# Optimization experiments

Hardware: AMD Instinct MI355X
Metric: run time of the kernel (lower is better)

Reference implementation:

```python
import jax, jax.numpy as jnp
import numpy as np

B, S, DIN, DOUT = 2, 2048, 4096, 4096


def setup_inputs() -> dict:
    key = jax.random.key(0)
    k1, k2 = jax.random.split(key)
    x = jax.random.normal(k1, (B, S, DIN), dtype=jnp.float32)
    weight = jax.random.normal(k2, (DOUT, DIN), dtype=jnp.float32) * 0.02
    # xnor init for row scaling pattern
    mean = weight.mean(-1, keepdims=True)                      # [DOUT,1]
    scale = jnp.abs(weight - mean).mean(-1, keepdims=True)     # [DOUT,1]
    wscale = scale
    wbias = mean
    return {"x": x, "weight": weight, "wscale": wscale, "wbias": wbias}


def reference(x, weight, wscale, wbias):
    # STE binarization: forward = sign(weight) (grad handled in bwd module)
    w_bin = jnp.sign(weight)
    w = wscale * w_bin + wbias                                 # [DOUT, DIN]
    # F.linear(x, w): x @ w.T, no bias
    out = jnp.einsum('bsk,nk->bsn', x, w)
    return out
```

## Files before the change

### kernel.cpp

```cpp
#include <hip/hip_runtime.h>
#include <stdint.h>


#define MDIM 4096
#define NDIM 4096
#define KDIM 4096

typedef int int4v __attribute__((ext_vector_type(4)));

__device__ __forceinline__ int pack4_rn(float a, float b, float c, float d, float inv) {
  int ia = __float2int_rn(a * inv) & 0xff;
  int ib = __float2int_rn(b * inv) & 0xff;
  int ic = __float2int_rn(c * inv) & 0xff;
  int id = __float2int_rn(d * inv) & 0xff;
  return ia | (ib << 8) | (ic << 16) | (id << 24);
}

__device__ __forceinline__ int sgn8(float v) {
  return (v > 0.f) ? 1 : ((v < 0.f) ? 0xff : 0);
}

__global__ __launch_bounds__(256) void prep_kernel(
    const float* __restrict__ x, const float* __restrict__ w,
    char* __restrict__ xq, char* __restrict__ wsg,
    float* __restrict__ xscale, float* __restrict__ sumx) {
  const int b = blockIdx.x;
  const int tid = threadIdx.x;
  if (b < MDIM) {
    const int row = b;
    const float4* xr = (const float4*)(x + (size_t)row * KDIM);
    float4 v[4];
    float s = 0.f, amax = 0.f;
#pragma unroll
    for (int u = 0; u < 4; ++u) {
      v[u] = xr[u * 256 + tid];
      s += v[u].x + v[u].y + v[u].z + v[u].w;
      amax = fmaxf(amax, fmaxf(fmaxf(fabsf(v[u].x), fabsf(v[u].y)),
                               fmaxf(fabsf(v[u].z), fabsf(v[u].w))));
    }
#pragma unroll
    for (int off = 32; off > 0; off >>= 1) {
      s += __shfl_down(s, off, 64);
      amax = fmaxf(amax, __shfl_down(amax, off, 64));
    }
    __shared__ float rs[4], rm[4], bcast;
    if ((tid & 63) == 0) { rs[tid >> 6] = s; rm[tid >> 6] = amax; }
    __syncthreads();
    if (tid == 0) {
      sumx[row] = rs[0] + rs[1] + rs[2] + rs[3];
      float mt = fmaxf(fmaxf(rm[0], rm[1]), fmaxf(rm[2], rm[3]));
      xscale[row] = mt * (1.f / 127.f);
      bcast = (mt > 0.f) ? 127.f / mt : 0.f;
    }
    __syncthreads();
    const float inv = bcast;
    int* xo = (int*)(xq + (size_t)row * KDIM);
#pragma unroll
    for (int u = 0; u < 4; ++u)
      xo[u * 256 + tid] = pack4_rn(v[u].x, v[u].y, v[u].z, v[u].w, inv);
  } else {
    const size_t base = (size_t)(b - MDIM) * (256 * 4);
    const float4* wr = (const float4*)w;
    int* wo = (int*)wsg;
#pragma unroll
    for (int u = 0; u < 4; ++u) {
      size_t i = base + u * 256 + tid;
      float4 v = wr[i];
      wo[i] = sgn8(v.x) | (sgn8(v.y) << 8) | (sgn8(v.z) << 16) | (sgn8(v.w) << 24);
    }
  }
}

__global__ __launch_bounds__(256) void gemm_bin_i8_kernel(
    const char* __restrict__ A, const char* __restrict__ Bs,
    const float* __restrict__ wscale, const float* __restrict__ wbias,
    const float* __restrict__ xscale, const float* __restrict__ sumx,
    float* __restrict__ C) {
  __shared__ __align__(16) char sA0[128 * 64], sA1[128 * 64], sA2[128 * 64];
  __shared__ __align__(16) char sB0[128 * 64], sB1[128 * 64], sB2[128 * 64];

  const int bn = blockIdx.x & 31;
  const int bm = blockIdx.x >> 5;
  const int tm0 = bm * 128, tn0 = bn * 128;
  const int tid = threadIdx.x;
  const int lane = tid & 63, wave = tid >> 6;
  const int quad = lane >> 4, l16 = lane & 15;
  const int wmo = (wave >> 1) * 64, wno = (wave & 1) * 64;

  int4v acc[4][4];
  const int4v zero4 = {0, 0, 0, 0};
#pragma unroll
  for (int i = 0; i < 4; ++i)
#pragma unroll
    for (int j = 0; j < 4; ++j) acc[i][j] = zero4;

  int st_row[2], st_lblk[2];
#pragma unroll
  for (int q = 0; q < 2; ++q) {
    int u = q * 256 + tid;
    st_row[q] = u >> 2;
    st_lblk[q] = (u & 3) ^ ((st_row[q] >> 1) & 3);
  }
  const char* gA0 = A  + (size_t)(tm0 + st_row[0]) * KDIM + st_lblk[0] * 16;
  const char* gA1 = A  + (size_t)(tm0 + st_row[1]) * KDIM + st_lblk[1] * 16;
  const char* gB0 = Bs + (size_t)(tn0 + st_row[0]) * KDIM + st_lblk[0] * 16;
  const char* gB1 = Bs + (size_t)(tn0 + st_row[1]) * KDIM + st_lblk[1] * 16;
  const int ld0 = tid * 16, ld1 = 4096 + tid * 16;

  int aOff[4], bOff[4];
#pragma unroll
  for (int i = 0; i < 4; ++i) {
    int r = wmo + i * 16 + l16;
    aOff[i] = r * 64 + (quad ^ ((r >> 1) & 3)) * 16;
  }
#pragma unroll
  for (int j = 0; j < 4; ++j) {
    int r = wno + j * 16 + l16;
    bOff[j] = r * 64 + (quad ^ ((r >> 1) & 3)) * 16;
  }

#define STAGE(dstA, dstB, kofs)                                                  \
  do {                                                                           \
    __builtin_amdgcn_global_load_lds(                                            \
        (const __attribute__((address_space(1))) void*)(gA0 + (kofs)),           \
        (__attribute__((address_space(3))) void*)((dstA) + ld0), 16, 0, 0);      \
    __builtin_amdgcn_global_load_lds(                                            \
        (const __attribute__((address_space(1))) void*)(gA1 + (kofs)),           \
        (__attribute__((address_space(3))) void*)((dstA) + ld1), 16, 0, 0);      \
    __builtin_amdgcn_global_load_lds(                                            \
        (const __attribute__((address_space(1))) void*)(gB0 + (kofs)),           \
        (__attribute__((address_space(3))) void*)((dstB) + ld0), 16, 0, 0);      \
    __builtin_amdgcn_global_load_lds(                                            \
        (const __attribute__((address_space(1))) void*)(gB1 + (kofs)),           \
        (__attribute__((address_space(3))) void*)((dstB) + ld1), 16, 0, 0);      \
  } while (0)

#define COMPUTE(srcA, srcB)                                                      \
  do {                                                                           \
    int4v af[4], bfr[4];                                                         \
    _Pragma("unroll") for (int i = 0; i < 4; ++i)                                \
        af[i] = *(const int4v*)((srcA) + aOff[i]);                               \
    _Pragma("unroll") for (int j = 0; j < 4; ++j)                                \
        bfr[j] = *(const int4v*)((srcB) + bOff[j]);                              \
    _Pragma("unroll") for (int i = 0; i < 4; ++i)                                \
        _Pragma("unroll") for (int j = 0; j < 4; ++j)                            \
            acc[i][j] = __builtin_amdgcn_mfma_i32_16x16x64_i8(af[i], bfr[j],     \
                                                              acc[i][j], 0, 0, 0);\
  } while (0)

#define SYNC_KEEP4() asm volatile("s_waitcnt vmcnt(4)\n\ts_barrier" ::: "memory")
#define SYNC_ALL()   asm volatile("s_waitcnt vmcnt(0)\n\ts_barrier" ::: "memory")

#define ITER(cA, cB, pA, pB, kofs_next)                                          \
  do {                                                                           \
    SYNC_KEEP4();                                                                \
    STAGE(pA, pB, (kofs_next));                                                  \
    COMPUTE(cA, cB);                                                             \
  } while (0)

  STAGE(sA0, sB0, 0);
  STAGE(sA1, sB1, 64);
  for (int i = 0; i < 60; i += 3) {
    ITER(sA0, sB0, sA2, sB2, (i + 2) * 64);
    ITER(sA1, sB1, sA0, sB0, (i + 3) * 64);
    ITER(sA2, sB2, sA1, sB1, (i + 4) * 64);
  }
  ITER(sA0, sB0, sA2, sB2, 62 * 64);
  ITER(sA1, sB1, sA0, sB0, 63 * 64);
  SYNC_KEEP4();
  COMPUTE(sA2, sB2);
  SYNC_ALL();
  COMPUTE(sA0, sB0);
#undef ITER
#undef SYNC_KEEP4
#undef SYNC_ALL
#undef STAGE
#undef COMPUTE

  float wsv[4], wbv[4];
#pragma unroll
  for (int j = 0; j < 4; ++j) {
    int n = tn0 + wno + j * 16 + l16;
    wsv[j] = wscale[n];
    wbv[j] = wbias[n];
  }
#pragma unroll
  for (int i = 0; i < 4; ++i) {
#pragma unroll
    for (int r = 0; r < 4; ++r) {
      int m = tm0 + wmo + i * 16 + quad * 4 + r;
      float xs = xscale[m];
      float sx = sumx[m];
      float* crow = C + (size_t)m * NDIM + tn0 + wno + l16;
#pragma unroll
      for (int j = 0; j < 4; ++j) {
        crow[j * 16] = wsv[j] * xs * (float)acc[i][j][r] + wbv[j] * sx;
      }
    }
  }
}

extern "C" void kernel_launch(void* const* d_in, const int* in_sizes, int n_in,
                              void* d_out, int out_size, void* d_ws, size_t ws_size,
                              hipStream_t stream) {
  const float* x      = (const float*)d_in[0];
  const float* weight = (const float*)d_in[1];
  const float* wscale = (const float*)d_in[2];
  const float* wbias  = (const float*)d_in[3];
  float* out = (float*)d_out;

  char* xq  = (char*)d_ws;
  char* wsg = xq + (size_t)MDIM * KDIM;
  float* xscale = (float*)(wsg + (size_t)NDIM * KDIM);
  float* sumx   = xscale + MDIM;

  prep_kernel<<<MDIM + (NDIM * KDIM) / (16 * 256), 256, 0, stream>>>(
      x, weight, xq, wsg, xscale, sumx);
  gemm_bin_i8_kernel<<<(MDIM / 128) * (NDIM / 128), 256, 0, stream>>>(
      xq, wsg, wscale, wbias, xscale, sumx, out);
}
```

Before: 244.4 us.

## Use 256x256 tiles with 8 waves and an 8-phase interleaved load/MFMA pipeline

The int8 GEMM moves from 128x128 tiles with 4 waves to 256x256 tiles with 8 waves and 128 KB of LDS. Each K-step of 128 is split into phases, and each phase issues the next half-tile global-to-LDS loads before running MFMAs under raised priority. It also uses a new LDS swizzle. The aim is more reuse per byte loaded and better overlap of memory with MFMA work. The cost is more barriers per K-step, only 256 blocks in total, and 128 KB LDS per block, which may allow only one block per CU despite launch_bounds(512,2).

```diff
diff --git a/kernel.cpp b/kernel.cpp
--- a/kernel.cpp
+++ b/kernel.cpp
@@ -71,130 +71,164 @@
   }
 }
 
-__global__ __launch_bounds__(256) void gemm_bin_i8_kernel(
+__global__ __launch_bounds__(512, 2) void gemm_bin_i8_8phase(
     const char* __restrict__ A, const char* __restrict__ Bs,
     const float* __restrict__ wscale, const float* __restrict__ wbias,
     const float* __restrict__ xscale, const float* __restrict__ sumx,
     float* __restrict__ C) {
-  __shared__ __align__(16) char sA0[128 * 64], sA1[128 * 64], sA2[128 * 64];
-  __shared__ __align__(16) char sB0[128 * 64], sB1[128 * 64], sB2[128 * 64];
-
-  const int bn = blockIdx.x & 31;
-  const int bm = blockIdx.x >> 5;
-  const int tm0 = bm * 128, tn0 = bn * 128;
+  __shared__ __align__(16) char sm[131072];
+
+  const int bm = blockIdx.x >> 4, bn = blockIdx.x & 15;
+  const int tm0 = bm * 256, tn0 = bn * 256;
   const int tid = threadIdx.x;
   const int lane = tid & 63, wave = tid >> 6;
   const int quad = lane >> 4, l16 = lane & 15;
-  const int wmo = (wave >> 1) * 64, wno = (wave & 1) * 64;
-
-  int4v acc[4][4];
+  const int wr = wave >> 2, wc = wave & 3;
+
+  int4v acc[2][4][4];
   const int4v zero4 = {0, 0, 0, 0};
 #pragma unroll
-  for (int i = 0; i < 4; ++i)
-#pragma unroll
-    for (int j = 0; j < 4; ++j) acc[i][j] = zero4;
-
-  int st_row[2], st_lblk[2];
-#pragma unroll
-  for (int q = 0; q < 2; ++q) {
-    int u = q * 256 + tid;
-    st_row[q] = u >> 2;
-    st_lblk[q] = (u & 3) ^ ((st_row[q] >> 1) & 3);
-  }
-  const char* gA0 = A  + (size_t)(tm0 + st_row[0]) * KDIM + st_lblk[0] * 16;
-  const char* gA1 = A  + (size_t)(tm0 + st_row[1]) * KDIM + st_lblk[1] * 16;
-  const char* gB0 = Bs + (size_t)(tn0 + st_row[0]) * KDIM + st_lblk[0] * 16;
-  const char* gB1 = Bs + (size_t)(tn0 + st_row[1]) * KDIM + st_lblk[1] * 16;
-  const int ld0 = tid * 16, ld1 = 4096 + tid * 16;
-
-  int aOff[4], bOff[4];
-#pragma unroll
-  for (int i = 0; i < 4; ++i) {
-    int r = wmo + i * 16 + l16;
-    aOff[i] = r * 64 + (quad ^ ((r >> 1) & 3)) * 16;
-  }
+  for (int rh = 0; rh < 2; ++rh)
+#pragma unroll
+    for (int i = 0; i < 4; ++i)
+#pragma unroll
+      for (int j = 0; j < 4; ++j) acc[rh][i][j] = zero4;
+
+  int4v bf[4];
+
+  int aOff[2][4];
+#pragma unroll
+  for (int rh = 0; rh < 2; ++rh)
+#pragma unroll
+    for (int i = 0; i < 4; ++i) {
+      int row = wr * 128 + rh * 64 + i * 16 + l16;
+      int sw = (row ^ (row >> 2)) & 3;
+      aOff[rh][i] = row * 64 + ((quad ^ sw) & 3) * 16;
+    }
+  int bOff[4];
 #pragma unroll
   for (int j = 0; j < 4; ++j) {
-    int r = wno + j * 16 + l16;
-    bOff[j] = r * 64 + (quad ^ ((r >> 1) & 3)) * 16;
-  }
-
-#define STAGE(dstA, dstB, kofs)                                                  \
-  do {                                                                           \
-    __builtin_amdgcn_global_load_lds(                                            \
-        (const __attribute__((address_space(1))) void*)(gA0 + (kofs)),           \
-        (__attribute__((address_space(3))) void*)((dstA) + ld0), 16, 0, 0);      \
-    __builtin_amdgcn_global_load_lds(                                            \
-        (const __attribute__((address_space(1))) void*)(gA1 + (kofs)),           \
-        (__attribute__((address_space(3))) void*)((dstA) + ld1), 16, 0, 0);      \
-    __builtin_amdgcn_global_load_lds(                                            \
-        (const __attribute__((address_space(1))) void*)(gB0 + (kofs)),           \
-        (__attribute__((address_space(3))) void*)((dstB) + ld0), 16, 0, 0);      \
-    __builtin_amdgcn_global_load_lds(                                            \
-        (const __attribute__((address_space(1))) void*)(gB1 + (kofs)),           \
-        (__attribute__((address_space(3))) void*)((dstB) + ld1), 16, 0, 0);      \
-  } while (0)
-
-#define COMPUTE(srcA, srcB)                                                      \
-  do {                                                                           \
-    int4v af[4], bfr[4];                                                         \
-    _Pragma("unroll") for (int i = 0; i < 4; ++i)                                \
-        af[i] = *(const int4v*)((srcA) + aOff[i]);                               \
-    _Pragma("unroll") for (int j = 0; j < 4; ++j)                                \
-        bfr[j] = *(const int4v*)((srcB) + bOff[j]);                              \
-    _Pragma("unroll") for (int i = 0; i < 4; ++i)                                \
-        _Pragma("unroll") for (int j = 0; j < 4; ++j)                            \
-            acc[i][j] = __builtin_amdgcn_mfma_i32_16x16x64_i8(af[i], bfr[j],     \
-                                                              acc[i][j], 0, 0, 0);\
-  } while (0)
-
-#define SYNC_KEEP4() asm volatile("s_waitcnt vmcnt(4)\n\ts_barrier" ::: "memory")
-#define SYNC_ALL()   asm volatile("s_waitcnt vmcnt(0)\n\ts_barrier" ::: "memory")
-
-#define ITER(cA, cB, pA, pB, kofs_next)                                          \
-  do {                                                                           \
-    SYNC_KEEP4();                                                                \
-    STAGE(pA, pB, (kofs_next));                                                  \
-    COMPUTE(cA, cB);                                                             \
-  } while (0)
-
-  STAGE(sA0, sB0, 0);
-  STAGE(sA1, sB1, 64);
-  for (int i = 0; i < 60; i += 3) {
-    ITER(sA0, sB0, sA2, sB2, (i + 2) * 64);
-    ITER(sA1, sB1, sA0, sB0, (i + 3) * 64);
-    ITER(sA2, sB2, sA1, sB1, (i + 4) * 64);
-  }
-  ITER(sA0, sB0, sA2, sB2, 62 * 64);
-  ITER(sA1, sB1, sA0, sB0, 63 * 64);
-  SYNC_KEEP4();
-  COMPUTE(sA2, sB2);
-  SYNC_ALL();
-  COMPUTE(sA0, sB0);
-#undef ITER
-#undef SYNC_KEEP4
-#undef SYNC_ALL
-#undef STAGE
-#undef COMPUTE
+    int row = wc * 64 + j * 16 + l16;
+    int sw = (row ^ (row >> 2)) & 3;
+    bOff[j] = 65536 + row * 64 + ((quad ^ sw) & 3) * 16;
+  }
+
+  const int u0 = tid, u1 = tid + 512;
+  const int r0 = u0 >> 2, r1 = u1 >> 2;
+  const int c0 = (u0 & 3) ^ ((r0 ^ (r0 >> 2)) & 3);
+  const int c1 = (u1 & 3) ^ ((r1 ^ (r1 >> 2)) & 3);
+  const char* gA0 = A + (size_t)(tm0 + r0) * KDIM + c0 * 16;
+  const char* gA1 = A + (size_t)(tm0 + r1) * KDIM + c1 * 16;
+  const char* gB0 = Bs + (size_t)(tn0 + r0) * KDIM + c0 * 16;
+  const char* gB1 = Bs + (size_t)(tn0 + r1) * KDIM + c1 * 16;
+  const int ldsu0 = tid * 16, ldsu1 = 8192 + tid * 16;
+
+#define STAGE_A(BUF, KH, KOFS)                                                    \
+  do {                                                                            \
+    const int base_ = ((BUF) * 2 + (KH)) * 16384;                                 \
+    __builtin_amdgcn_global_load_lds(                                             \
+        (const __attribute__((address_space(1))) void*)(gA0 + (KOFS)),            \
+        (__attribute__((address_space(3))) void*)(sm + base_ + ldsu0), 16, 0, 0); \
+    __builtin_amdgcn_global_load_lds(                                             \
+        (const __attribute__((address_space(1))) void*)(gA1 + (KOFS)),            \
+        (__attribute__((address_space(3))) void*)(sm + base_ + ldsu1), 16, 0, 0); \
+  } while (0)
+
+#define STAGE_B(BUF, KH, KOFS)                                                    \
+  do {                                                                            \
+    const int base_ = 65536 + ((BUF) * 2 + (KH)) * 16384;                         \
+    __builtin_amdgcn_global_load_lds(                                             \
+        (const __attribute__((address_space(1))) void*)(gB0 + (KOFS)),            \
+        (__attribute__((address_space(3))) void*)(sm + base_ + ldsu0), 16, 0, 0); \
+    __builtin_amdgcn_global_load_lds(                                             \
+        (const __attribute__((address_space(1))) void*)(gB1 + (KOFS)),            \
+        (__attribute__((address_space(3))) void*)(sm + base_ + ldsu1), 16, 0, 0); \
+  } while (0)
+
+#define BAR __builtin_amdgcn_s_barrier()
+#define CK4 asm volatile("s_waitcnt vmcnt(4)\n\ts_barrier" ::: "memory")
+#define CK0 asm volatile("s_waitcnt vmcnt(0)\n\ts_barrier" ::: "memory")
+
+#define PHASE(BUF, KS, RH, CKBAR, ...)                                            \
+  do {                                                                            \
+    int4v af[4];                                                                  \
+    _Pragma("unroll") for (int i_ = 0; i_ < 4; ++i_)                              \
+        af[i_] = *(const int4v*)(sm + ((BUF) * 2 + (KS)) * 16384 + aOff[RH][i_]); \
+    if ((RH) == 0) {                                                              \
+      _Pragma("unroll") for (int j_ = 0; j_ < 4; ++j_)                            \
+          bf[j_] = *(const int4v*)(sm + ((BUF) * 2 + (KS)) * 16384 + bOff[j_]);   \
+    }                                                                             \
+    __VA_ARGS__;                                                                  \
+    __builtin_amdgcn_s_barrier();                                                 \
+    asm volatile("s_waitcnt lgkmcnt(0)" ::: "memory");                            \
+    __builtin_amdgcn_sched_barrier(0);                                            \
+    __builtin_amdgcn_s_setprio(1);                                                \
+    _Pragma("unroll") for (int i_ = 0; i_ < 4; ++i_)                              \
+        _Pragma("unroll") for (int j_ = 0; j_ < 4; ++j_)                          \
+            acc[RH][i_][j_] = __builtin_amdgcn_mfma_i32_16x16x64_i8(              \
+                af[i_], bf[j_], acc[RH][i_][j_], 0, 0, 0);                        \
+    __builtin_amdgcn_s_setprio(0);                                                \
+    CKBAR;                                                                        \
+  } while (0)
+
+#define ITER_FULL(BUF, TAU)                                                       \
+  do {                                                                            \
+    PHASE(BUF, 0, 0, BAR, STAGE_A((BUF) ^ 1, 1, ((TAU) + 1) * 128 + 64));         \
+    PHASE(BUF, 0, 1, BAR, STAGE_B((BUF) ^ 1, 1, ((TAU) + 1) * 128 + 64));         \
+    PHASE(BUF, 1, 0, BAR, STAGE_A(BUF, 0, ((TAU) + 2) * 128));                    \
+    PHASE(BUF, 1, 1, CK4, STAGE_B(BUF, 0, ((TAU) + 2) * 128));                    \
+  } while (0)
+
+  STAGE_A(0, 0, 0);
+  STAGE_B(0, 0, 0);
+  STAGE_A(0, 1, 64);
+  STAGE_B(0, 1, 64);
+  STAGE_A(1, 0, 128);
+  STAGE_B(1, 0, 128);
+  CK4;
+
+#pragma unroll 1
+  for (int t = 0; t < 30; t += 2) {
+    ITER_FULL(0, t);
+    ITER_FULL(1, t + 1);
+  }
+  PHASE(0, 0, 0, BAR, STAGE_A(1, 1, 31 * 128 + 64));
+  PHASE(0, 0, 1, BAR, STAGE_B(1, 1, 31 * 128 + 64));
+  PHASE(0, 1, 0, BAR, (void)0);
+  PHASE(0, 1, 1, CK0, (void)0);
+  PHASE(1, 0, 0, BAR, (void)0);
+  PHASE(1, 0, 1, BAR, (void)0);
+  PHASE(1, 1, 0, BAR, (void)0);
+  PHASE(1, 1, 1, BAR, (void)0);
+
+#undef ITER_FULL
+#undef PHASE
+#undef BAR
+#undef CK4
+#undef CK0
+#undef STAGE_A
+#undef STAGE_B
 
   float wsv[4], wbv[4];
 #pragma unroll
   for (int j = 0; j < 4; ++j) {
-    int n = tn0 + wno + j * 16 + l16;
+    int n = tn0 + wc * 64 + j * 16 + l16;
     wsv[j] = wscale[n];
     wbv[j] = wbias[n];
   }
 #pragma unroll
-  for (int i = 0; i < 4; ++i) {
-#pragma unroll
-    for (int r = 0; r < 4; ++r) {
-      int m = tm0 + wmo + i * 16 + quad * 4 + r;
-      float xs = xscale[m];
-      float sx = sumx[m];
-      float* crow = C + (size_t)m * NDIM + tn0 + wno + l16;
-#pragma unroll
-      for (int j = 0; j < 4; ++j) {
-        crow[j * 16] = wsv[j] * xs * (float)acc[i][j][r] + wbv[j] * sx;
+  for (int rh = 0; rh < 2; ++rh) {
+#pragma unroll
+    for (int i = 0; i < 4; ++i) {
+#pragma unroll
+      for (int r = 0; r < 4; ++r) {
+        int m = tm0 + wr * 128 + rh * 64 + i * 16 + quad * 4 + r;
+        float xs = xscale[m];
+        float sx = sumx[m];
+        float* crow = C + (size_t)m * NDIM + tn0 + wc * 64 + l16;
+#pragma unroll
+        for (int j = 0; j < 4; ++j)
+          crow[j * 16] = wsv[j] * xs * (float)acc[rh][i][j][r] + wbv[j] * sx;
       }
     }
   }
@@ -216,6 +250,6 @@
 
   prep_kernel<<<MDIM + (NDIM * KDIM) / (16 * 256), 256, 0, stream>>>(
       x, weight, xq, wsg, xscale, sumx);
-  gemm_bin_i8_kernel<<<(MDIM / 128) * (NDIM / 128), 256, 0, stream>>>(
+  gemm_bin_i8_8phase<<<(MDIM / 256) * (NDIM / 256), 512, 0, stream>>>(
       xq, wsg, wscale, wbias, xscale, sumx, out);
 }
```

Measured after the change: 234.7 us. 1.04x faster.
